# Kernel tuning notes

Measured on AMD Instinct MI355X. Metric: run time of the kernel, lower is better.

Reference implementation:

```python
import jax, jax.numpy as jnp
import numpy as np

B, N, D = 8, 1024, 1024
H, DH = 16, 64
INNER = H * DH  # == D by construction
MLP = 4096
EPS = 1e-5


def layernorm(x, g, b):
    mu = jnp.mean(x, axis=-1, keepdims=True)
    var = jnp.mean(jnp.square(x - mu), axis=-1, keepdims=True)
    return (x - mu) * jax.lax.rsqrt(var + EPS) * g + b


def setup_inputs() -> dict:
    key = jax.random.key(0)
    ks = jax.random.split(key, 10)
    s = lambda fan_in: 1.0 / np.sqrt(fan_in)
    return {
        "x": jax.random.normal(ks[0], (B, N, D), jnp.float32),
        "ln1_g": jnp.ones((D,), jnp.float32),
        "ln1_b": jnp.zeros((D,), jnp.float32),
        "w_qkv": jax.random.uniform(ks[1], (D, 3 * INNER), jnp.float32, -s(D), s(D)),
        "w_out": jax.random.uniform(ks[2], (INNER, D), jnp.float32, -s(INNER), s(INNER)),
        "b_out": jnp.zeros((D,), jnp.float32),
        "ln2_g": jnp.ones((D,), jnp.float32),
        "ln2_b": jnp.zeros((D,), jnp.float32),
        "w1": jax.random.uniform(ks[3], (D, MLP), jnp.float32, -s(D), s(D)),
        "b1": jnp.zeros((MLP,), jnp.float32),
        "w2": jax.random.uniform(ks[4], (MLP, D), jnp.float32, -s(MLP), s(MLP)),
        "b2": jnp.zeros((D,), jnp.float32),
    }


def reference(x, ln1_g, ln1_b, w_qkv, w_out, b_out, ln2_g, ln2_b, w1, b1, w2, b2):
    scale = DH ** -0.5
    xn = layernorm(x, ln1_g, ln1_b)
    qkv = xn @ w_qkv  # [B, N, 3*INNER]
    embed_dim = xn.shape[-1]
    # faithful to source: slice by embed_dim (== INNER here)
    q, k, v = (qkv[:, :, embed_dim * i: embed_dim * (i + 1)] for i in range(3))
    reshape_heads = lambda t: t.reshape(B, N, H, DH).transpose(0, 2, 1, 3)  # b h n d
    q, k, v = reshape_heads(q), reshape_heads(k), reshape_heads(v)
    scores = jnp.einsum("bhnd,bhmd->bhnm", q, k) * scale
    attn = jax.nn.softmax(scores, axis=-1)
    attn_out = jnp.einsum("bhnm,bhmd->bhnd", attn, v)
    attn_out = attn_out.transpose(0, 2, 1, 3).reshape(B, N, INNER)
    x2 = attn_out @ w_out + b_out  # to_ff projection (project_out=True)
    # feed_forward: LayerNorm -> Linear -> GELU(exact) -> Linear (dropout=0)
    h = layernorm(x2, ln2_g, ln2_b) @ w1 + b1
    h = jax.nn.gelu(h, approximate=False)
    out = h @ w2 + b2
    return out
```

## Files before the change

kernel.cpp:

```cpp
#include <hip/hip_runtime.h>
#include <hip/hip_bf16.h>
#include <math.h>

typedef __bf16 bf16;
typedef __bf16 bf16x4 __attribute__((ext_vector_type(4)));
typedef __bf16 bf16x8 __attribute__((ext_vector_type(8)));
typedef float f32x4 __attribute__((ext_vector_type(4)));

#define SEQ 1024
#define DMODEL 1024

__device__ __forceinline__ void gld_lds16(const bf16* g, bf16* l) {
    __builtin_amdgcn_global_load_lds(
        (const __attribute__((address_space(1))) unsigned int*)g,
        (__attribute__((address_space(3))) unsigned int*)l, 16, 0, 0);
}

__global__ void transpose_f2b(const float* __restrict__ in, bf16* __restrict__ out,
                              int K, int N) {
    __shared__ float tile[32][33];
    int n0 = blockIdx.x * 32, k0 = blockIdx.y * 32;
    int tx = threadIdx.x, ty = threadIdx.y;
#pragma unroll
    for (int i = 0; i < 4; ++i) {
        int kk = ty + i * 8;
        tile[kk][tx] = in[(size_t)(k0 + kk) * N + n0 + tx];
    }
    __syncthreads();
#pragma unroll
    for (int i = 0; i < 4; ++i) {
        int nn = ty + i * 8;
        out[(size_t)(n0 + nn) * K + k0 + tx] = (bf16)tile[tx][nn];
    }
}

__global__ void ln_f2b(const float* __restrict__ x, const float* __restrict__ g,
                       const float* __restrict__ bta, bf16* __restrict__ y) {
    int row = blockIdx.x, t = threadIdx.x;
    const float* xr = x + (size_t)row * DMODEL;
    float v[4];
#pragma unroll
    for (int i = 0; i < 4; ++i) v[i] = xr[t * 4 + i];
    float s = v[0] + v[1] + v[2] + v[3];
    float s2 = v[0] * v[0] + v[1] * v[1] + v[2] * v[2] + v[3] * v[3];
#pragma unroll
    for (int off = 32; off > 0; off >>= 1) {
        s += __shfl_down(s, off, 64);
        s2 += __shfl_down(s2, off, 64);
    }
    __shared__ float ws1[4], ws2[4];
    __shared__ float mu_s, rstd_s;
    int lane = t & 63, wv = t >> 6;
    if (lane == 0) { ws1[wv] = s; ws2[wv] = s2; }
    __syncthreads();
    if (t == 0) {
        float S1 = ws1[0] + ws1[1] + ws1[2] + ws1[3];
        float S2 = ws2[0] + ws2[1] + ws2[2] + ws2[3];
        float mu = S1 * (1.0f / DMODEL);
        float var = S2 * (1.0f / DMODEL) - mu * mu;
        mu_s = mu;
        rstd_s = rsqrtf(var + 1e-5f);
    }
    __syncthreads();
    float mu = mu_s, rstd = rstd_s;
    bf16* yr = y + (size_t)row * DMODEL;
#pragma unroll
    for (int i = 0; i < 4; ++i) {
        int d = t * 4 + i;
        float o = (v[i] - mu) * rstd * g[d] + bta[d];
        yr[d] = (bf16)o;
    }
}

#define BM 128
#define BN 128
#define BK 32

__global__ __launch_bounds__(256, 2) void gemm_bt(
    const bf16* __restrict__ A, const bf16* __restrict__ Bt,
    const float* __restrict__ bias, void* __restrict__ Cv,
    int M, int N, int K, int mode) {
    __shared__ bf16 sA[BM * BK];
    __shared__ bf16 sB[BN * BK];
    int t = threadIdx.x;
    int lane = t & 63, wave = t >> 6;
    int wr = wave >> 1, wc = wave & 1;
    int m0 = blockIdx.y * BM, n0 = blockIdx.x * BN;
    const bf16* Ap = A + (size_t)m0 * K;
    const bf16* Bp = Bt + (size_t)n0 * K;

    int srow = wave * 16 + (lane >> 2);
    int schunk = lane & 3;
    int gcoff = (schunk ^ (srow & 3)) * 8;
    const bf16* gA0 = Ap + (size_t)srow * K + gcoff;
    const bf16* gA1 = Ap + (size_t)(srow + 64) * K + gcoff;
    const bf16* gB0 = Bp + (size_t)srow * K + gcoff;
    const bf16* gB1 = Bp + (size_t)(srow + 64) * K + gcoff;
    bf16* lA0 = sA + wave * 512;
    bf16* lA1 = sA + 2048 + wave * 512;
    bf16* lB0 = sB + wave * 512;
    bf16* lB1 = sB + 2048 + wave * 512;

    f32x4 acc[4][4];
#pragma unroll
    for (int i = 0; i < 4; ++i)
#pragma unroll
        for (int j = 0; j < 4; ++j) acc[i][j] = (f32x4){0.f, 0.f, 0.f, 0.f};

    int mq = lane & 15, quad = lane >> 4;
    int csw = (quad ^ (mq & 3)) * 8;

    for (int k0 = 0; k0 < K; k0 += BK) {
        __syncthreads();
        gld_lds16(gA0 + k0, lA0);
        gld_lds16(gA1 + k0, lA1);
        gld_lds16(gB0 + k0, lB0);
        gld_lds16(gB1 + k0, lB1);
        __syncthreads();
        bf16x8 af[4], bfr[4];
#pragma unroll
        for (int i = 0; i < 4; ++i)
            af[i] = *(const bf16x8*)&sA[(wr * 64 + i * 16 + mq) * BK + csw];
#pragma unroll
        for (int j = 0; j < 4; ++j)
            bfr[j] = *(const bf16x8*)&sB[(wc * 64 + j * 16 + mq) * BK + csw];
#pragma unroll
        for (int i = 0; i < 4; ++i)
#pragma unroll
            for (int j = 0; j < 4; ++j)
                acc[i][j] = __builtin_amdgcn_mfma_f32_16x16x32_bf16(af[i], bfr[j], acc[i][j], 0, 0, 0);
    }

    int cq = lane & 15, rq = (lane >> 4) * 4;
#pragma unroll
    for (int i = 0; i < 4; ++i) {
        int row = m0 + wr * 64 + i * 16 + rq;
#pragma unroll
        for (int j = 0; j < 4; ++j) {
            int col = n0 + wc * 64 + j * 16 + cq;
            float bv = bias ? bias[col] : 0.0f;
#pragma unroll
            for (int r = 0; r < 4; ++r) {
                float v = acc[i][j][r] + bv;
                if (mode == 1) v = 0.5f * v * (1.0f + erff(v * 0.70710678118654752f));
                size_t idx = (size_t)(row + r) * N + col;
                if (mode == 2) ((float*)Cv)[idx] = v;
                else           ((bf16*)Cv)[idx] = (bf16)v;
            }
        }
    }
}

#define KVB 128
#define LDK2 72
#define LDP 136

__global__ __launch_bounds__(256, 2) void attn_mfma(const bf16* __restrict__ qkv,
                                                    bf16* __restrict__ ao) {
    __shared__ bf16 Klds[KVB][LDK2];
    __shared__ bf16 Vtlds[64][LDP];
    __shared__ bf16 Plds[4][16][LDP];
    int t = threadIdx.x, lane = t & 63, wave = t >> 6;

    int f = (int)blockIdx.y * (int)gridDim.x + (int)blockIdx.x;
    int wg = (f & 7) * 256 + (f >> 3);
    int bh = wg >> 4, bb = bh >> 4, h = bh & 15;
    int q0 = (wg & 15) * 64;

    const bf16* base = qkv + (size_t)bb * SEQ * 3072;
    int m = lane & 15, quad = lane >> 4;
    int kq = quad * 8;

    bf16x8 qf[2];
    {
        int qrow = q0 + wave * 16 + m;
        const bf16* p = base + (size_t)qrow * 3072 + h * 64;
#pragma unroll
        for (int c = 0; c < 2; ++c) {
            bf16x8 tmp = *(const bf16x8*)(p + c * 32 + kq);
#pragma unroll
            for (int j = 0; j < 8; ++j) qf[c][j] = (bf16)((float)tmp[j] * 0.125f);
        }
    }

    float m_run = -3e38f, l_run = 0.f;
    f32x4 o_acc[4];
#pragma unroll
    for (int g = 0; g < 4; ++g) o_acc[g] = (f32x4){0.f, 0.f, 0.f, 0.f};

    int skey = t >> 3, sd0 = (t & 7) * 8;
    int rot = t & 7;
    const bf16* pk0 = base + (size_t)skey * 3072 + 1024 + h * 64 + sd0;
    const bf16* pv0 = base + (size_t)skey * 3072 + 2048 + h * 64 + sd0;

    bf16x8 kreg[4], vreg[4];

#define LOADKV(kt2) do { \
    const bf16* pk = pk0 + (size_t)(kt2) * KVB * 3072; \
    const bf16* pv = pv0 + (size_t)(kt2) * KVB * 3072; \
    _Pragma("unroll") for (int c = 0; c < 4; ++c) { \
        kreg[c] = *(const bf16x8*)(pk + (size_t)c * 32 * 3072); \
        vreg[c] = *(const bf16x8*)(pv + (size_t)c * 32 * 3072); } \
} while (0)
#define WRITEKV() do { \
    _Pragma("unroll") for (int c = 0; c < 4; ++c) { \
        *(bf16x8*)&Klds[skey + c * 32][sd0] = kreg[c]; \
        _Pragma("unroll") for (int ii = 0; ii < 8; ++ii) { \
            int j = (ii + rot) & 7; \
            Vtlds[sd0 + j][skey + c * 32] = vreg[c][j]; } } \
} while (0)

    LOADKV(0);
    WRITEKV();
    __syncthreads();

    for (int kt = 0; kt < SEQ / KVB; ++kt) {
        if (kt + 1 < SEQ / KVB) LOADKV(kt + 1);

        f32x4 s[8];
#pragma unroll
        for (int g = 0; g < 8; ++g) {
            bf16x8 b0 = *(const bf16x8*)&Klds[g * 16 + m][kq];
            bf16x8 b1 = *(const bf16x8*)&Klds[g * 16 + m][32 + kq];
            s[g] = (f32x4){0.f, 0.f, 0.f, 0.f};
            s[g] = __builtin_amdgcn_mfma_f32_16x16x32_bf16(b0, qf[0], s[g], 0, 0, 0);
            s[g] = __builtin_amdgcn_mfma_f32_16x16x32_bf16(b1, qf[1], s[g], 0, 0, 0);
        }

        {
            float mx = s[0][0];
#pragma unroll
            for (int g = 0; g < 8; ++g)
#pragma unroll
                for (int r = 0; r < 4; ++r) mx = fmaxf(mx, s[g][r]);
            mx = fmaxf(mx, __shfl_xor(mx, 16, 64));
            mx = fmaxf(mx, __shfl_xor(mx, 32, 64));
            float m_new = fmaxf(m_run, mx);
            float alpha = __expf(m_run - m_new);
            m_run = m_new;
            float rs = 0.f;
#pragma unroll
            for (int g = 0; g < 8; ++g)
#pragma unroll
                for (int r = 0; r < 4; ++r) {
                    float p = __expf(s[g][r] - m_new);
                    s[g][r] = p;
                    rs += p;
                }
            rs += __shfl_xor(rs, 16, 64);
            rs += __shfl_xor(rs, 32, 64);
            l_run = l_run * alpha + rs;
            float av[4];
#pragma unroll
            for (int r = 0; r < 4; ++r) av[r] = __shfl(alpha, quad * 4 + r, 64);
#pragma unroll
            for (int g = 0; g < 4; ++g)
#pragma unroll
                for (int r = 0; r < 4; ++r) o_acc[g][r] *= av[r];
        }

#pragma unroll
        for (int g = 0; g < 8; ++g) {
            bf16x4 pw = {(bf16)s[g][0], (bf16)s[g][1], (bf16)s[g][2], (bf16)s[g][3]};
            *(bf16x4*)&Plds[wave][m][g * 16 + quad * 4] = pw;
        }

#pragma unroll
        for (int kc = 0; kc < 4; ++kc) {
            bf16x8 pf = *(const bf16x8*)&Plds[wave][m][kc * 32 + kq];
#pragma unroll
            for (int dg = 0; dg < 4; ++dg) {
                bf16x8 vf = *(const bf16x8*)&Vtlds[dg * 16 + m][kc * 32 + kq];
                o_acc[dg] = __builtin_amdgcn_mfma_f32_16x16x32_bf16(pf, vf, o_acc[dg], 0, 0, 0);
            }
        }

        __syncthreads();
        if (kt + 1 < SEQ / KVB) {
            WRITEKV();
        }
        __syncthreads();
    }

#undef LOADKV
#undef WRITEKV

#pragma unroll
    for (int r = 0; r < 4; ++r) {
        int row = q0 + wave * 16 + quad * 4 + r;
        float rl = 1.0f / __shfl(l_run, quad * 4 + r, 64);
        bf16* op = ao + ((size_t)bb * SEQ + row) * DMODEL + h * 64;
#pragma unroll
        for (int g = 0; g < 4; ++g) op[g * 16 + m] = (bf16)(o_acc[g][r] * rl);
    }
}

extern "C" void kernel_launch(void* const* d_in, const int* in_sizes, int n_in,
                              void* d_out, int out_size, void* d_ws, size_t ws_size,
                              hipStream_t stream) {
    const float* x     = (const float*)d_in[0];
    const float* ln1_g = (const float*)d_in[1];
    const float* ln1_b = (const float*)d_in[2];
    const float* w_qkv = (const float*)d_in[3];
    const float* w_out = (const float*)d_in[4];
    const float* b_out = (const float*)d_in[5];
    const float* ln2_g = (const float*)d_in[6];
    const float* ln2_b = (const float*)d_in[7];
    const float* w1    = (const float*)d_in[8];
    const float* b1    = (const float*)d_in[9];
    const float* w2    = (const float*)d_in[10];
    const float* b2    = (const float*)d_in[11];
    float* out = (float*)d_out;
    char* ws = (char*)d_ws;
    char* outc = (char*)d_out;

    bf16* wqkvT = (bf16*)(ws + (0ull << 20));
    bf16* woutT = (bf16*)(ws + (6ull << 20));
    bf16* qkv   = (bf16*)(ws + (8ull << 20));
    bf16* w1T   = (bf16*)(ws + (8ull << 20));
    bf16* w2T   = (bf16*)(ws + (16ull << 20));
    float* x2   = (float*)(ws + (24ull << 20));
    bf16* hbuf  = (bf16*)(ws + (24ull << 20));
    bf16* xn    = (bf16*)(outc + 0);
    bf16* ao    = (bf16*)(outc + 0);
    bf16* x2n   = (bf16*)(outc + (16ull << 20));

    dim3 tb(32, 8);
    transpose_f2b<<<dim3(3072 / 32, 1024 / 32), tb, 0, stream>>>(w_qkv, wqkvT, 1024, 3072);
    transpose_f2b<<<dim3(1024 / 32, 1024 / 32), tb, 0, stream>>>(w_out, woutT, 1024, 1024);

    ln_f2b<<<8192, 256, 0, stream>>>(x, ln1_g, ln1_b, xn);
    gemm_bt<<<dim3(3072 / 128, 8192 / 128), 256, 0, stream>>>(xn, wqkvT, nullptr, qkv,
                                                              8192, 3072, 1024, 0);
    attn_mfma<<<dim3(SEQ / 64, 128), 256, 0, stream>>>(qkv, ao);

    transpose_f2b<<<dim3(4096 / 32, 1024 / 32), tb, 0, stream>>>(w1, w1T, 1024, 4096);
    transpose_f2b<<<dim3(1024 / 32, 4096 / 32), tb, 0, stream>>>(w2, w2T, 4096, 1024);

    gemm_bt<<<dim3(1024 / 128, 8192 / 128), 256, 0, stream>>>(ao, woutT, b_out, x2,
                                                              8192, 1024, 1024, 2);
    ln_f2b<<<8192, 256, 0, stream>>>(x2, ln2_g, ln2_b, x2n);

    for (int c = 0; c < 2; ++c) {
        const bf16* a1 = x2n + (size_t)c * 4096 * 1024;
        float* oc = out + (size_t)c * 4096 * 1024;
        gemm_bt<<<dim3(4096 / 128, 4096 / 128), 256, 0, stream>>>(a1, w1T, b1, hbuf,
                                                                  4096, 4096, 1024, 1);
        gemm_bt<<<dim3(1024 / 128, 4096 / 128), 256, 0, stream>>>(hbuf, w2T, b2, oc,
                                                                  4096, 1024, 4096, 2);
    }
}
```

Baseline: 623.6 us.

## Keep attention probabilities in registers via transposed PV MFMA, drop P LDS

The attention kernel now computes the output transposed (V^T times P), so the probability fragments produced by the QK^T MFMA feed straight into a 16x16x16 bf16 MFMA. This removes the per-wave LDS round-trip for P and the alpha/l shuffles. It also folds log2(e) into the Q scale so exp2f replaces __expf, and raises the launch-bounds occupancy target from 2 to 4 blocks. The trade-off is twice as many, smaller MFMAs for PV and possible register pressure or spills at the higher occupancy target.

```diff
diff --git a/kernel.cpp b/kernel.cpp
--- a/kernel.cpp
+++ b/kernel.cpp
@@ -5,6 +5,7 @@
 typedef __bf16 bf16;
 typedef __bf16 bf16x4 __attribute__((ext_vector_type(4)));
 typedef __bf16 bf16x8 __attribute__((ext_vector_type(8)));
+typedef short s16x4 __attribute__((ext_vector_type(4)));
 typedef float f32x4 __attribute__((ext_vector_type(4)));
 
 #define SEQ 1024
@@ -14,6 +15,16 @@
     __builtin_amdgcn_global_load_lds(
         (const __attribute__((address_space(1))) unsigned int*)g,
         (__attribute__((address_space(3))) unsigned int*)l, 16, 0, 0);
+}
+
+__device__ __forceinline__ f32x4 mfma16_bf16(bf16x4 a, bf16x4 b, f32x4 c) {
+#if __has_builtin(__builtin_amdgcn_mfma_f32_16x16x16_bf16)
+    return __builtin_amdgcn_mfma_f32_16x16x16_bf16(a, b, c, 0, 0, 0);
+#else
+    union { bf16x4 h; s16x4 i; } ua, ub;
+    ua.h = a; ub.h = b;
+    return __builtin_amdgcn_mfma_f32_16x16x16bf16_1k(ua.i, ub.i, c, 0, 0, 0);
+#endif
 }
 
 __global__ void transpose_f2b(const float* __restrict__ in, bf16* __restrict__ out,
@@ -155,11 +166,10 @@
 #define LDK2 72
 #define LDP 136
 
-__global__ __launch_bounds__(256, 2) void attn_mfma(const bf16* __restrict__ qkv,
+__global__ __launch_bounds__(256, 4) void attn_mfma(const bf16* __restrict__ qkv,
                                                     bf16* __restrict__ ao) {
     __shared__ bf16 Klds[KVB][LDK2];
     __shared__ bf16 Vtlds[64][LDP];
-    __shared__ bf16 Plds[4][16][LDP];
     int t = threadIdx.x, lane = t & 63, wave = t >> 6;
 
     int f = (int)blockIdx.y * (int)gridDim.x + (int)blockIdx.x;
@@ -179,14 +189,15 @@
         for (int c = 0; c < 2; ++c) {
             bf16x8 tmp = *(const bf16x8*)(p + c * 32 + kq);
 #pragma unroll
-            for (int j = 0; j < 8; ++j) qf[c][j] = (bf16)((float)tmp[j] * 0.125f);
+            for (int j = 0; j < 8; ++j)
+                qf[c][j] = (bf16)((float)tmp[j] * 0.18033688011112042f);
         }
     }
 
     float m_run = -3e38f, l_run = 0.f;
-    f32x4 o_acc[4];
-#pragma unroll
-    for (int g = 0; g < 4; ++g) o_acc[g] = (f32x4){0.f, 0.f, 0.f, 0.f};
+    f32x4 o_accT[4];
+#pragma unroll
+    for (int dg = 0; dg < 4; ++dg) o_accT[dg] = (f32x4){0.f, 0.f, 0.f, 0.f};
 
     int skey = t >> 3, sd0 = (t & 7) * 8;
     int rot = t & 7;
@@ -228,52 +239,49 @@
         }
 
         {
-            float mx = s[0][0];
+            float mg[8];
 #pragma unroll
             for (int g = 0; g < 8; ++g)
-#pragma unroll
-                for (int r = 0; r < 4; ++r) mx = fmaxf(mx, s[g][r]);
+                mg[g] = fmaxf(fmaxf(s[g][0], s[g][1]), fmaxf(s[g][2], s[g][3]));
+            float mx = fmaxf(fmaxf(fmaxf(mg[0], mg[1]), fmaxf(mg[2], mg[3])),
+                             fmaxf(fmaxf(mg[4], mg[5]), fmaxf(mg[6], mg[7])));
             mx = fmaxf(mx, __shfl_xor(mx, 16, 64));
             mx = fmaxf(mx, __shfl_xor(mx, 32, 64));
             float m_new = fmaxf(m_run, mx);
-            float alpha = __expf(m_run - m_new);
+            float alpha = exp2f(m_run - m_new);
             m_run = m_new;
             float rs = 0.f;
 #pragma unroll
             for (int g = 0; g < 8; ++g)
 #pragma unroll
                 for (int r = 0; r < 4; ++r) {
-                    float p = __expf(s[g][r] - m_new);
+                    float p = exp2f(s[g][r] - m_new);
                     s[g][r] = p;
                     rs += p;
                 }
             rs += __shfl_xor(rs, 16, 64);
             rs += __shfl_xor(rs, 32, 64);
             l_run = l_run * alpha + rs;
-            float av[4];
-#pragma unroll
-            for (int r = 0; r < 4; ++r) av[r] = __shfl(alpha, quad * 4 + r, 64);
-#pragma unroll
-            for (int g = 0; g < 4; ++g)
-#pragma unroll
-                for (int r = 0; r < 4; ++r) o_acc[g][r] *= av[r];
-        }
-
+#pragma unroll
+            for (int dg = 0; dg < 4; ++dg)
+#pragma unroll
+                for (int r = 0; r < 4; ++r) o_accT[dg][r] *= alpha;
+        }
+
+        bf16x4 pb[8];
 #pragma unroll
         for (int g = 0; g < 8; ++g) {
-            bf16x4 pw = {(bf16)s[g][0], (bf16)s[g][1], (bf16)s[g][2], (bf16)s[g][3]};
-            *(bf16x4*)&Plds[wave][m][g * 16 + quad * 4] = pw;
-        }
-
-#pragma unroll
-        for (int kc = 0; kc < 4; ++kc) {
-            bf16x8 pf = *(const bf16x8*)&Plds[wave][m][kc * 32 + kq];
+            bf16x4 w = {(bf16)s[g][0], (bf16)s[g][1], (bf16)s[g][2], (bf16)s[g][3]};
+            pb[g] = w;
+        }
+
+#pragma unroll
+        for (int g = 0; g < 8; ++g)
 #pragma unroll
             for (int dg = 0; dg < 4; ++dg) {
-                bf16x8 vf = *(const bf16x8*)&Vtlds[dg * 16 + m][kc * 32 + kq];
-                o_acc[dg] = __builtin_amdgcn_mfma_f32_16x16x32_bf16(pf, vf, o_acc[dg], 0, 0, 0);
+                bf16x4 va = *(const bf16x4*)&Vtlds[dg * 16 + m][g * 16 + quad * 4];
+                o_accT[dg] = mfma16_bf16(va, pb[g], o_accT[dg]);
             }
-        }
 
         __syncthreads();
         if (kt + 1 < SEQ / KVB) {
@@ -285,13 +293,16 @@
 #undef LOADKV
 #undef WRITEKV
 
-#pragma unroll
-    for (int r = 0; r < 4; ++r) {
-        int row = q0 + wave * 16 + quad * 4 + r;
-        float rl = 1.0f / __shfl(l_run, quad * 4 + r, 64);
+    {
+        float rl = 1.0f / l_run;
+        int row = q0 + wave * 16 + m;
         bf16* op = ao + ((size_t)bb * SEQ + row) * DMODEL + h * 64;
 #pragma unroll
-        for (int g = 0; g < 4; ++g) op[g * 16 + m] = (bf16)(o_acc[g][r] * rl);
+        for (int dg = 0; dg < 4; ++dg) {
+            bf16x4 ov = {(bf16)(o_accT[dg][0] * rl), (bf16)(o_accT[dg][1] * rl),
+                         (bf16)(o_accT[dg][2] * rl), (bf16)(o_accT[dg][3] * rl)};
+            *(bf16x4*)&op[dg * 16 + quad * 4] = ov;
+        }
     }
 }
 
```

New measurement: 637.9 us. +2.3%, slower.
